# Optimization experiments

Hardware: AMD Instinct MI355X
Metric: run time of the kernel (lower is better)

## Reference

```python
import jax, jax.numpy as jnp
import numpy as np

B, N, E = 32, 2048, 4096
D_IN, C, H = 256, 64, 4          # node_hidden_size, gnn_hidden_size, num_heads
SLOPE = 0.2                       # PyG GATConv default negative_slope


def gat_conv(x, src, dst, W, att_src, att_dst, bias):
    """One PyG-style GATConv (concat=True, add_self_loops=True) on a single graph.
    x: [N, Din]; src/dst: [E] int; W: [Din, H*C]; att_*: [H, C]; bias: [H*C]."""
    n = x.shape[0]
    h = (x @ W).reshape(n, H, C)                       # [N,H,C]
    a_src = jnp.einsum('nhc,hc->nh', h, att_src)       # [N,H]
    a_dst = jnp.einsum('nhc,hc->nh', h, att_dst)
    loop = jnp.arange(n, dtype=src.dtype)              # self loops
    s = jnp.concatenate([src, loop])
    d = jnp.concatenate([dst, loop])
    e = jax.nn.leaky_relu(a_src[s] + a_dst[d], SLOPE)  # [E+N,H]
    # segment softmax over incoming edges of each target node
    m = jax.ops.segment_max(e, d, num_segments=n)
    ex = jnp.exp(e - m[d])
    denom = jax.ops.segment_sum(ex, d, num_segments=n)
    alpha = ex / (denom[d] + 1e-16)                    # [E+N,H]
    out = jax.ops.segment_sum(alpha[:, :, None] * h[s], d, num_segments=n)  # [N,H,C]
    return out.reshape(n, H * C) + bias


def setup_inputs() -> dict:
    key = jax.random.key(0)
    ks = jax.random.split(key, 12)
    g = lambda k, shp, fan: jax.random.normal(k, shp, jnp.float32) * (1.0 / np.sqrt(fan))
    return {
        'node_embeddings': jax.random.normal(ks[0], (B, N, D_IN), jnp.float32),
        'src_index': jax.random.randint(ks[1], (B, E), 0, N, jnp.int32),
        'tgt_index': jax.random.randint(ks[2], (B, E), 0, N, jnp.int32),
        'W1': g(ks[3], (D_IN, H * C), D_IN),
        'att_src1': g(ks[4], (H, C), C),
        'att_dst1': g(ks[5], (H, C), C),
        'bias1': jnp.zeros((H * C,), jnp.float32),
        'W2': g(ks[6], (H * C, H * C), H * C),
        'att_src2': g(ks[7], (H, C), C),
        'att_dst2': g(ks[8], (H, C), C),
        'bias2': jnp.zeros((H * C,), jnp.float32),
    }


def reference(node_embeddings, src_index, tgt_index, W1, att_src1, att_dst1, bias1,
              W2, att_src2, att_dst2, bias2):
    def per_graph(x, s, d):
        m = gat_conv(x, s, d, W1, att_src1, att_dst1, bias1)
        m = jax.nn.elu(m)                              # dropout = identity (eval)
        m = gat_conv(m, s, d, W2, att_src2, att_dst2, bias2)
        return m
    return jax.vmap(per_graph)(node_embeddings, src_index, tgt_index)  # [B,N,H*C]
```

## Files before the change

kernel.cpp:

```cpp
#include <hip/hip_runtime.h>
#include <hip/hip_bf16.h>
#include <cstdint>

#define BB 32
#define NN 2048
#define EE 4096
#define HH 4
#define CC 64
#define DD 256
#define MM (BB*NN)

typedef __attribute__((ext_vector_type(8))) short bf16x8;
typedef __attribute__((ext_vector_type(8))) unsigned short u16x8;
typedef __attribute__((ext_vector_type(4))) float f32x4;

__device__ __forceinline__ float b2f(__hip_bfloat16 x){ return __bfloat162float(x); }
__device__ __forceinline__ float u2f(unsigned short u){ return __uint_as_float((unsigned)u << 16); }
__device__ __forceinline__ unsigned short f2u(float f){
  __hip_bfloat16 h = __float2bfloat16(f);
  return *(unsigned short*)&h;
}
__device__ __forceinline__ float ldany(const void* p, int isf, size_t i){
  return isf ? ((const float*)p)[i] : b2f(((const __hip_bfloat16*)p)[i]);
}
__device__ __forceinline__ void gld_lds16(const void* g, void* l){
  __builtin_amdgcn_global_load_lds((const __attribute__((address_space(1))) uint32_t*)g,
                                   (__attribute__((address_space(3))) uint32_t*)l, 16, 0, 0);
}

__global__ void detect_kernel(const unsigned* __restrict__ w, int* __restrict__ flag){
  __shared__ int cnt;
  if(threadIdx.x == 0) cnt = 0;
  __syncthreads();
  int c = 0;
  #pragma unroll
  for(int i = 0; i < 4; ++i){
    unsigned v = w[threadIdx.x*4 + i];
    unsigned elo = (v >> 7) & 0xFFu;
    if(elo >= 100u && elo <= 150u) ++c;
  }
  atomicAdd(&cnt, c);
  __syncthreads();
  if(threadIdx.x == 0) *flag = (cnt < 128) ? 1 : 0;
}

__global__ __launch_bounds__(256) void convX_kernel(const void* __restrict__ src,
    unsigned short* __restrict__ dst, const int* __restrict__ flag){
  int isf = *flag;
  int blk  = blockIdx.x;
  int vblk = (blk & 7)*2048 + (blk >> 3);
  size_t i = ((size_t)vblk*256 + threadIdx.x)*4;
  ushort4 o;
  if(isf){
    float4 v = *(const float4*)((const float*)src + i);
    o.x = f2u(v.x); o.y = f2u(v.y); o.z = f2u(v.z); o.w = f2u(v.w);
  } else {
    o = *(const ushort4*)((const unsigned short*)src + i);
  }
  *(ushort4*)(dst + i) = o;
}
__global__ __launch_bounds__(256) void convWT_kernel(const void* __restrict__ W,
    __hip_bfloat16* __restrict__ WT, const int* __restrict__ flag){
  int isf = *flag;
  int i = blockIdx.x*256 + threadIdx.x;
  WT[i] = __float2bfloat16(ldany(W, isf, (size_t)(i & 255)*256 + (i >> 8)));
}
__global__ __launch_bounds__(256) void conv6_kernel(const void* s0, const void* s1,
    const void* s2, const void* s3, const void* s4, const void* s5,
    float* __restrict__ dst, const int* __restrict__ flag){
  int isf = *flag;
  int i = blockIdx.x*256 + threadIdx.x;
  int seg = i >> 8, off = i & 255;
  const void* s = seg==0?s0 : seg==1?s1 : seg==2?s2 : seg==3?s3 : seg==4?s4 : s5;
  dst[i] = ldany(s, isf, off);
}

__global__ __launch_bounds__(256) void mfma_gemm(const __hip_bfloat16* __restrict__ A,
    const __hip_bfloat16* __restrict__ BT, __hip_bfloat16* __restrict__ C,
    const float* __restrict__ attS, const float* __restrict__ attD,
    float* __restrict__ aS, float* __restrict__ aD)
{
  __shared__ __align__(16) short lds[128*128];
  short* lA = lds;
  short* lB = lds + 128*64;
  const int tid  = threadIdx.x;
  const int w    = tid >> 6, lane = tid & 63;
  const int dd   = blockIdx.x;
  const int xcd  = dd & 7, slot = dd >> 3;
  const int rb   = xcd*64 + (slot >> 1), cb = slot & 1;
  const int row0 = rb*128, col0 = cb*128;
  const int wr   = (w & 1)*64, wc = (w >> 1)*64;
  const int lr   = lane >> 3;
  const int kb_g = (lane & 7) ^ lr;
  const int fm   = lane & 15, quad = lane >> 4;
  f32x4 acc[4][4] = {};

  for(int k0 = 0; k0 < 256; k0 += 64){
    #pragma unroll
    for(int c = 0; c < 4; ++c){
      int ra = w*32 + c*8;
      const short* ga = (const short*)A  + (size_t)(row0 + ra + lr)*DD + k0 + kb_g*8;
      const short* gb = (const short*)BT + (size_t)(col0 + ra + lr)*DD + k0 + kb_g*8;
      gld_lds16(ga, &lA[ra*64]);
      gld_lds16(gb, &lB[ra*64]);
    }
    __syncthreads();
    #pragma unroll
    for(int ks = 0; ks < 2; ++ks){
      bf16x8 af[4], bfr[4];
      int kb = ks*4 + quad;
      #pragma unroll
      for(int i = 0; i < 4; ++i){
        int m = wr + i*16 + fm;
        af[i]  = *(const bf16x8*)&lA[m*64 + ((kb ^ (m & 7))*8)];
        int n = wc + i*16 + fm;
        bfr[i] = *(const bf16x8*)&lB[n*64 + ((kb ^ (n & 7))*8)];
      }
      #pragma unroll
      for(int i = 0; i < 4; ++i)
        #pragma unroll
        for(int j = 0; j < 4; ++j)
          acc[i][j] = __builtin_amdgcn_mfma_f32_16x16x32_bf16(af[i], bfr[j], acc[i][j], 0, 0, 0);
    }
    __syncthreads();
  }

  const int headI = (col0 + wc) >> 6;
  float ws_[4], wd_[4];
  #pragma unroll
  for(int j = 0; j < 4; ++j){
    ws_[j] = attS[headI*CC + j*16 + fm];
    wd_[j] = attD[headI*CC + j*16 + fm];
  }
  #pragma unroll
  for(int i = 0; i < 4; ++i){
    #pragma unroll
    for(int r = 0; r < 4; ++r){
      float s = 0.f, dv = 0.f;
      #pragma unroll
      for(int j = 0; j < 4; ++j){
        float v = acc[i][j][r];
        s  += v * ws_[j];
        dv += v * wd_[j];
      }
      #pragma unroll
      for(int m = 1; m <= 8; m <<= 1){
        s  += __shfl_xor(s,  m);
        dv += __shfl_xor(dv, m);
      }
      if(fm == i*4 + r){
        int row = row0 + wr + i*16 + quad*4 + r;
        aS[(size_t)row*HH + headI] = s;
        aD[(size_t)row*HH + headI] = dv;
      }
    }
  }

  #pragma unroll
  for(int i = 0; i < 4; ++i)
    #pragma unroll
    for(int j = 0; j < 4; ++j)
      #pragma unroll
      for(int r = 0; r < 4; ++r){
        int rl = wr + i*16 + quad*4 + r;
        int cl = wc + j*16 + fm;
        lds[rl*128 + (cl ^ ((rl & 12) << 2))] = (short)f2u(acc[i][j][r]);
      }
  __syncthreads();
  const int rr = tid >> 4, cc = (tid & 15)*8;
  #pragma unroll
  for(int p = 0; p < 8; ++p){
    int rl = p*16 + rr;
    u16x8 v = *(const u16x8*)&lds[rl*128 + (cc ^ ((rl & 12) << 2))];
    *(u16x8*)((unsigned short*)C + (size_t)(row0 + rl)*DD + col0 + cc) = v;
  }
}

__global__ __launch_bounds__(256) void deg_kernel(const int* __restrict__ dst, int* __restrict__ degc)
{
  int idx = blockIdx.x*256 + threadIdx.x;
  if(idx >= BB*EE) return;
  int b = idx >> 12;
  atomicAdd(&degc[b*NN + dst[idx]], 1);
}

__global__ __launch_bounds__(256) void scan_kernel(int* __restrict__ degc, int* __restrict__ row_ptr)
{
  __shared__ int part[256];
  int b = blockIdx.x, t = threadIdx.x;
  int loc[8], s = 0;
  #pragma unroll
  for(int i = 0; i < 8; ++i){ loc[i] = s; s += degc[b*NN + t*8 + i]; }
  part[t] = s;
  __syncthreads();
  if(t == 0){
    int run = 0;
    for(int i = 0; i < 256; ++i){ int tmp = part[i]; part[i] = run; run += tmp; }
  }
  __syncthreads();
  int base = b*EE + part[t];
  #pragma unroll
  for(int i = 0; i < 8; ++i){
    int v = base + loc[i];
    row_ptr[b*(NN+1) + t*8 + i] = v;
    degc   [b*NN     + t*8 + i] = v;
  }
  if(t == 255) row_ptr[b*(NN+1) + NN] = base + s;
}

__global__ __launch_bounds__(256) void scatter_kernel(const int* __restrict__ src,
    const int* __restrict__ dst, int* __restrict__ cursor, unsigned short* __restrict__ srcList)
{
  int idx = blockIdx.x*256 + threadIdx.x;
  if(idx >= BB*EE) return;
  int b = idx >> 12;
  int pos = atomicAdd(&cursor[b*NN + dst[idx]], 1);
  srcList[pos] = (unsigned short)src[idx];
}

template<int LAYER>
__global__ __launch_bounds__(256) void gather_kernel(const __hip_bfloat16* __restrict__ H,
    const float* __restrict__ a_src, const float* __restrict__ a_dst,
    const int* __restrict__ row_ptr, const unsigned short* __restrict__ srcList,
    const float* __restrict__ bias, void* __restrict__ outp,
    const int* __restrict__ flag)
{
  int blk  = blockIdx.x;
  int vblk = (blk & 7)*2048 + (blk >> 3);
  int wid  = vblk*4 + (int)(threadIdx.x >> 6);
  int lane = threadIdx.x & 63;
  int b = wid >> 11, d = wid & (NN-1);
  int head = lane >> 4;
  int start = row_ptr[b*(NN+1) + d];
  int end   = row_ptr[b*(NN+1) + d + 1];
  const unsigned short* Hu = (const unsigned short*)H;

  float adv = a_dst[wid*HH + head];
  float sv  = a_src[wid*HH + head] + adv;
  sv = sv > 0.f ? sv : 0.2f*sv;
  float exs = __expf(sv);

  ushort4 hv = *(const ushort4*)(Hu + (size_t)wid*DD + lane*4);
  f32x4 acc;
  acc.x = exs*u2f(hv.x); acc.y = exs*u2f(hv.y); acc.z = exs*u2f(hv.z); acc.w = exs*u2f(hv.w);
  float den = exs;

  int e = start;
  int s = 0; float ax = 0.f;
  if(e < end){ s = srcList[e]; ax = a_src[(b*NN + s)*HH + head]; }
  while(e < end){
    int sn = 0; float axn = 0.f;
    if(e + 1 < end){ sn = srcList[e+1]; axn = a_src[(b*NN + sn)*HH + head]; }
    float v = ax + adv;
    v = v > 0.f ? v : 0.2f*v;
    float ex = __expf(v);
    ushort4 hw = *(const ushort4*)(Hu + (size_t)(b*NN + s)*DD + lane*4);
    acc.x += ex*u2f(hw.x); acc.y += ex*u2f(hw.y); acc.z += ex*u2f(hw.z); acc.w += ex*u2f(hw.w);
    den += ex;
    s = sn; ax = axn; ++e;
  }
  float inv = 1.f / (den + 1e-16f);
  float4 bs = *(const float4*)(bias + lane*4);
  float o0 = acc.x*inv + bs.x, o1 = acc.y*inv + bs.y;
  float o2 = acc.z*inv + bs.z, o3 = acc.w*inv + bs.w;
  size_t oi = (size_t)wid*DD + lane*4;
  if(LAYER == 1){
    o0 = o0 > 0.f ? o0 : expm1f(o0);
    o1 = o1 > 0.f ? o1 : expm1f(o1);
    o2 = o2 > 0.f ? o2 : expm1f(o2);
    o3 = o3 > 0.f ? o3 : expm1f(o3);
    ushort4 ov = { f2u(o0), f2u(o1), f2u(o2), f2u(o3) };
    *(ushort4*)((unsigned short*)outp + oi) = ov;
  } else {
    if(*flag){
      float4 ov = { o0, o1, o2, o3 };
      *(float4*)((float*)outp + oi) = ov;
    } else {
      ushort4 ov = { f2u(o0), f2u(o1), f2u(o2), f2u(o3) };
      *(ushort4*)((unsigned short*)outp + oi) = ov;
    }
  }
}

extern "C" void kernel_launch(void* const* d_in, const int* in_sizes, int n_in,
                              void* d_out, int out_size, void* d_ws, size_t ws_size,
                              hipStream_t stream)
{
  const void* x_in = d_in[0];
  const int*  srcI = (const int*)d_in[1];
  const int*  dstI = (const int*)d_in[2];
  const void* W1   = d_in[3];
  const void* as1  = d_in[4];
  const void* ad1  = d_in[5];
  const void* b1   = d_in[6];
  const void* W2   = d_in[7];
  const void* as2  = d_in[8];
  const void* ad2  = d_in[9];
  const void* b2   = d_in[10];

  char* ws = (char*)d_ws;
  __hip_bfloat16* R1  = (__hip_bfloat16*)ws; ws += (size_t)MM*DD*2;
  __hip_bfloat16* R2  = (__hip_bfloat16*)ws; ws += (size_t)MM*DD*2;
  float* a_src = (float*)ws; ws += (size_t)MM*HH*4;
  float* a_dst = (float*)ws; ws += (size_t)MM*HH*4;
  __hip_bfloat16* W1t = (__hip_bfloat16*)ws; ws += (size_t)DD*DD*2;
  __hip_bfloat16* W2t = (__hip_bfloat16*)ws; ws += (size_t)DD*DD*2;
  float* attf = (float*)ws; ws += 1536*4;
  int*   degc = (int*)ws;   ws += (size_t)BB*NN*4;
  int*   rowp = (int*)ws;   ws += (size_t)BB*(NN+1)*4;
  unsigned short* srcL = (unsigned short*)ws; ws += (size_t)BB*EE*2;
  int*   flag = (int*)ws;   ws += 8;

  const int gemmBlocks   = (MM/128)*(DD/128);
  const int edgeBlocks   = (BB*EE)/256;
  const int gatherBlocks = (MM*64)/256;

  hipMemsetAsync(degc, 0, (size_t)BB*NN*4, stream);
  detect_kernel<<<1, 64, 0, stream>>>((const unsigned*)x_in, flag);
  convWT_kernel<<<DD*DD/256, 256, 0, stream>>>(W1, W1t, flag);
  convWT_kernel<<<DD*DD/256, 256, 0, stream>>>(W2, W2t, flag);
  conv6_kernel<<<6, 256, 0, stream>>>(as1, ad1, b1, as2, ad2, b2, attf, flag);
  convX_kernel<<<(int)(((size_t)MM*DD)/1024), 256, 0, stream>>>(x_in, (unsigned short*)R1, flag);

  deg_kernel    <<<edgeBlocks, 256, 0, stream>>>(dstI, degc);
  scan_kernel   <<<BB,         256, 0, stream>>>(degc, rowp);
  scatter_kernel<<<edgeBlocks, 256, 0, stream>>>(srcI, dstI, degc, srcL);

  mfma_gemm<<<gemmBlocks, 256, 0, stream>>>(R1, W1t, R2, attf + 0, attf + 256, a_src, a_dst);
  gather_kernel<1><<<gatherBlocks, 256, 0, stream>>>(R2, a_src, a_dst, rowp, srcL,
                                                     attf + 512, R1, flag);
  mfma_gemm<<<gemmBlocks, 256, 0, stream>>>(R1, W2t, R2, attf + 768, attf + 1024, a_src, a_dst);
  gather_kernel<2><<<gatherBlocks, 256, 0, stream>>>(R2, a_src, a_dst, rowp, srcL,
                                                     attf + 1280, d_out, flag);
}
```

Baseline: 255.1 us.

## Fuse fp32 input conversion into first GEMM and merge prep kernels

Removes the standalone pass that converted the fp32 node embeddings to bf16 into a workspace buffer. The first GEMM now reads fp32 rows directly, converts them in registers and writes swizzled bf16 into LDS. The weight transposes, attention-vector copies and degree-counter zeroing are merged into one prep kernel, replacing three launches and a memset. The cost is that the first GEMM's A-tile load becomes synchronous register-staged loads instead of direct global-to-LDS copies, and it reads twice as many bytes per tile.

```diff
diff --git a/kernel.cpp b/kernel.cpp
--- a/kernel.cpp
+++ b/kernel.cpp
@@ -44,45 +44,42 @@
   if(threadIdx.x == 0) *flag = (cnt < 128) ? 1 : 0;
 }
 
-__global__ __launch_bounds__(256) void convX_kernel(const void* __restrict__ src,
-    unsigned short* __restrict__ dst, const int* __restrict__ flag){
+__global__ __launch_bounds__(256) void prep_kernel(const void* __restrict__ W1,
+    const void* __restrict__ W2, __hip_bfloat16* __restrict__ W1t,
+    __hip_bfloat16* __restrict__ W2t,
+    const void* s0, const void* s1, const void* s2, const void* s3,
+    const void* s4, const void* s5, float* __restrict__ attf,
+    int* __restrict__ degc, const int* __restrict__ flag)
+{
   int isf = *flag;
-  int blk  = blockIdx.x;
-  int vblk = (blk & 7)*2048 + (blk >> 3);
-  size_t i = ((size_t)vblk*256 + threadIdx.x)*4;
-  ushort4 o;
-  if(isf){
-    float4 v = *(const float4*)((const float*)src + i);
-    o.x = f2u(v.x); o.y = f2u(v.y); o.z = f2u(v.z); o.w = f2u(v.w);
+  int bid = blockIdx.x, t = threadIdx.x;
+  if(bid < 512){
+    const void* W = (bid < 256) ? W1 : W2;
+    __hip_bfloat16* WT = (bid < 256) ? W1t : W2t;
+    int i = (bid & 255)*256 + t;
+    WT[i] = __float2bfloat16(ldany(W, isf, (size_t)(i & 255)*256 + (i >> 8)));
+  } else if(bid < 518){
+    int i = (bid - 512)*256 + t;
+    int seg = i >> 8, off = i & 255;
+    const void* s = seg==0?s0 : seg==1?s1 : seg==2?s2 : seg==3?s3 : seg==4?s4 : s5;
+    attf[i] = ldany(s, isf, off);
   } else {
-    o = *(const ushort4*)((const unsigned short*)src + i);
-  }
-  *(ushort4*)(dst + i) = o;
-}
-__global__ __launch_bounds__(256) void convWT_kernel(const void* __restrict__ W,
-    __hip_bfloat16* __restrict__ WT, const int* __restrict__ flag){
-  int isf = *flag;
-  int i = blockIdx.x*256 + threadIdx.x;
-  WT[i] = __float2bfloat16(ldany(W, isf, (size_t)(i & 255)*256 + (i >> 8)));
-}
-__global__ __launch_bounds__(256) void conv6_kernel(const void* s0, const void* s1,
-    const void* s2, const void* s3, const void* s4, const void* s5,
-    float* __restrict__ dst, const int* __restrict__ flag){
-  int isf = *flag;
-  int i = blockIdx.x*256 + threadIdx.x;
-  int seg = i >> 8, off = i & 255;
-  const void* s = seg==0?s0 : seg==1?s1 : seg==2?s2 : seg==3?s3 : seg==4?s4 : s5;
-  dst[i] = ldany(s, isf, off);
-}
-
-__global__ __launch_bounds__(256) void mfma_gemm(const __hip_bfloat16* __restrict__ A,
+    int i = (bid - 518)*256 + t;
+    int4 z = {0,0,0,0};
+    *((int4*)degc + i) = z;
+  }
+}
+
+template<int DYNA>
+__global__ __launch_bounds__(256) void mfma_gemm(const void* __restrict__ Ap,
     const __hip_bfloat16* __restrict__ BT, __hip_bfloat16* __restrict__ C,
     const float* __restrict__ attS, const float* __restrict__ attD,
-    float* __restrict__ aS, float* __restrict__ aD)
+    float* __restrict__ aS, float* __restrict__ aD, const int* __restrict__ flag)
 {
   __shared__ __align__(16) short lds[128*128];
   short* lA = lds;
   short* lB = lds + 128*64;
+  const int isf  = DYNA ? *flag : 0;
   const int tid  = threadIdx.x;
   const int w    = tid >> 6, lane = tid & 63;
   const int dd   = blockIdx.x;
@@ -99,10 +96,36 @@
     #pragma unroll
     for(int c = 0; c < 4; ++c){
       int ra = w*32 + c*8;
-      const short* ga = (const short*)A  + (size_t)(row0 + ra + lr)*DD + k0 + kb_g*8;
       const short* gb = (const short*)BT + (size_t)(col0 + ra + lr)*DD + k0 + kb_g*8;
-      gld_lds16(ga, &lA[ra*64]);
       gld_lds16(gb, &lB[ra*64]);
+    }
+    if(DYNA && isf){
+      const float* Af = (const float*)Ap;
+      float4 ta[4], tb[4];
+      #pragma unroll
+      for(int i = 0; i < 4; ++i){
+        int f8 = i*256 + tid;
+        int m = f8 >> 3, kb = f8 & 7;
+        const float* p = Af + (size_t)(row0 + m)*DD + k0 + kb*8;
+        ta[i] = *(const float4*)p;
+        tb[i] = *(const float4*)(p + 4);
+      }
+      #pragma unroll
+      for(int i = 0; i < 4; ++i){
+        int f8 = i*256 + tid;
+        int m = f8 >> 3, kb = f8 & 7;
+        u16x8 o;
+        o[0] = f2u(ta[i].x); o[1] = f2u(ta[i].y); o[2] = f2u(ta[i].z); o[3] = f2u(ta[i].w);
+        o[4] = f2u(tb[i].x); o[5] = f2u(tb[i].y); o[6] = f2u(tb[i].z); o[7] = f2u(tb[i].w);
+        *(u16x8*)&lA[m*64 + ((kb ^ (m & 7))*8)] = o;
+      }
+    } else {
+      #pragma unroll
+      for(int c = 0; c < 4; ++c){
+        int ra = w*32 + c*8;
+        const short* ga = (const short*)Ap + (size_t)(row0 + ra + lr)*DD + k0 + kb_g*8;
+        gld_lds16(ga, &lA[ra*64]);
+      }
     }
     __syncthreads();
     #pragma unroll
@@ -315,21 +338,20 @@
   const int edgeBlocks   = (BB*EE)/256;
   const int gatherBlocks = (MM*64)/256;
 
-  hipMemsetAsync(degc, 0, (size_t)BB*NN*4, stream);
   detect_kernel<<<1, 64, 0, stream>>>((const unsigned*)x_in, flag);
-  convWT_kernel<<<DD*DD/256, 256, 0, stream>>>(W1, W1t, flag);
-  convWT_kernel<<<DD*DD/256, 256, 0, stream>>>(W2, W2t, flag);
-  conv6_kernel<<<6, 256, 0, stream>>>(as1, ad1, b1, as2, ad2, b2, attf, flag);
-  convX_kernel<<<(int)(((size_t)MM*DD)/1024), 256, 0, stream>>>(x_in, (unsigned short*)R1, flag);
+  prep_kernel<<<582, 256, 0, stream>>>(W1, W2, W1t, W2t,
+                                       as1, ad1, b1, as2, ad2, b2, attf, degc, flag);
 
   deg_kernel    <<<edgeBlocks, 256, 0, stream>>>(dstI, degc);
   scan_kernel   <<<BB,         256, 0, stream>>>(degc, rowp);
   scatter_kernel<<<edgeBlocks, 256, 0, stream>>>(srcI, dstI, degc, srcL);
 
-  mfma_gemm<<<gemmBlocks, 256, 0, stream>>>(R1, W1t, R2, attf + 0, attf + 256, a_src, a_dst);
+  mfma_gemm<1><<<gemmBlocks, 256, 0, stream>>>(x_in, W1t, R2, attf + 0, attf + 256,
+                                               a_src, a_dst, flag);
   gather_kernel<1><<<gatherBlocks, 256, 0, stream>>>(R2, a_src, a_dst, rowp, srcL,
                                                      attf + 512, R1, flag);
-  mfma_gemm<<<gemmBlocks, 256, 0, stream>>>(R1, W2t, R2, attf + 768, attf + 1024, a_src, a_dst);
+  mfma_gemm<0><<<gemmBlocks, 256, 0, stream>>>(R1, W2t, R2, attf + 768, attf + 1024,
+                                               a_src, a_dst, flag);
   gather_kernel<2><<<gatherBlocks, 256, 0, stream>>>(R2, a_src, a_dst, rowp, srcL,
                                                      attf + 1280, d_out, flag);
 }
```

New measurement: 242.6 us. 4.9% less time.
